# Kernel optimization log

Measured on AMD Instinct MI355X. Metric: run time of the kernel, lower is better.

Reference implementation:

```python
import jax, jax.numpy as jnp
import numpy as np

TAU_MEM = 0.02
THRESHOLD = 0.5
RESET_POTENTIAL = 0.0
SURROGATE_BETA = 4.0
LN_EPS = 1e-6

B, T, F_IN, F_OUT = 64, 1024, 512, 512


def fast_sigmoid(x, beta):
    # Continuous fast-sigmoid surrogate spike: 0.5 * (beta*x / (1 + beta*|x|)) + 0.5
    bx = beta * x
    return 0.5 * bx / (1.0 + jnp.abs(bx)) + 0.5


def setup_inputs() -> dict:
    key = jax.random.key(0)
    k1, k2, k3 = jax.random.split(key, 3)
    spikes = jax.random.uniform(k1, (B, T, F_IN), dtype=jnp.float32)
    W = jax.random.normal(k2, (F_IN, F_OUT), dtype=jnp.float32) / np.sqrt(F_IN)
    b = jnp.zeros((F_OUT,), dtype=jnp.float32)
    ln_scale = jnp.ones((F_OUT,), dtype=jnp.float32)
    ln_bias = jnp.zeros((F_OUT,), dtype=jnp.float32)
    return {"spikes": spikes, "W": W, "b": b, "ln_scale": ln_scale, "ln_bias": ln_bias}


def reference(spikes, W, b, ln_scale, ln_bias):
    # Dense projection of input spike trains: [B,T,F_in] -> [B,T,F_out]
    currents = jnp.einsum('bti,io->bto', spikes, W) + b

    alpha = jnp.exp(jnp.float32(-1.0 / TAU_MEM))

    def lif_step(v_mem, cur):
        v_mem = alpha * v_mem + (1.0 - alpha) * cur
        spike = fast_sigmoid(v_mem - THRESHOLD, SURROGATE_BETA)
        v_mem = v_mem * (1.0 - spike) + RESET_POTENTIAL * spike
        return v_mem, spike

    v0 = jnp.zeros((spikes.shape[0], W.shape[1]), dtype=currents.dtype)
    _, out = jax.lax.scan(lif_step, v0, jnp.transpose(currents, (1, 0, 2)))  # [T,B,F]
    out = jnp.transpose(out, (1, 0, 2))  # [B,T,F]

    # LayerNorm over last axis (flax defaults: eps=1e-6, scale & bias)
    mean = jnp.mean(out, axis=-1, keepdims=True)
    var = jnp.var(out, axis=-1, keepdims=True)
    out = (out - mean) * jax.lax.rsqrt(var + LN_EPS) * ln_scale + ln_bias
    return out
```

## Files before the change

kernel.cpp:

```cpp
#include <hip/hip_runtime.h>

#define THREADS 1024
#define NBLK 512
#define BUFSZ 49152

typedef _Float16 half8 __attribute__((ext_vector_type(8)));
typedef float floatx4 __attribute__((ext_vector_type(4)));

__global__ void wcvt_kernel(const float* __restrict__ W, unsigned short* __restrict__ Wt) {
  __shared__ float tile[32][33];
  const int tx = threadIdx.x, ty = threadIdx.y;
  const int nb = blockIdx.x * 32, kb = blockIdx.y * 32;
#pragma unroll
  for (int i = 0; i < 4; ++i)
    tile[ty + 8 * i][tx] = W[(size_t)(kb + ty + 8 * i) * 512 + nb + tx];
  __syncthreads();
#pragma unroll
  for (int i = 0; i < 4; ++i) {
    union { _Float16 h; unsigned short u; } v;
    v.h = (_Float16)tile[tx][ty + 8 * i];
    Wt[(size_t)(nb + ty + 8 * i) * 512 + kb + tx] = v.u;
  }
}

__global__ __launch_bounds__(THREADS, 4) void lif_fused_kernel(
    const float* __restrict__ A, const unsigned short* __restrict__ Wt,
    const float* __restrict__ bias, const float* __restrict__ lnw,
    const float* __restrict__ lnb, float* __restrict__ out) {
  __shared__ uint4 smem4[9216];
  unsigned char* smem = (unsigned char*)smem4;

  const int tid  = threadIdx.x;
  const int lane = tid & 63;
  const int wave = tid >> 6;
  const int wrow = wave >> 2;
  const int wcol = wave & 3;
  const int l15  = lane & 15;
  const int g    = lane >> 4;
  const int rowBase = blockIdx.x * 128;

  const int arow = tid >> 3;
  const float* asrc =
      A + (size_t)(rowBase + arow) * 512 + ((tid & 7) ^ (arow & 7)) * 4;
  const int brow = tid >> 2;
  const unsigned short* bsrc =
      Wt + (size_t)brow * 512 + ((tid & 3) ^ (brow & 3) ^ ((brow >> 2) & 3)) * 8;

  auto stage = [&](int buf, int c) {
    int offA = buf * BUFSZ + wave * 1024;
    offA = __builtin_amdgcn_readfirstlane(offA);
    __builtin_amdgcn_global_load_lds(
        (const __attribute__((address_space(1))) void*)(asrc + c * 32),
        (__attribute__((address_space(3))) void*)(smem + offA), 16, 0, 0);
    int offB = buf * BUFSZ + 16384 + wave * 1024;
    offB = __builtin_amdgcn_readfirstlane(offB);
    __builtin_amdgcn_global_load_lds(
        (const __attribute__((address_space(1))) void*)(bsrc + c * 32),
        (__attribute__((address_space(3))) void*)(smem + offB), 16, 0, 0);
    __builtin_amdgcn_global_load_lds(
        (const __attribute__((address_space(1))) void*)(bsrc + 256 * 512 + c * 32),
        (__attribute__((address_space(3))) void*)(smem + offB + 16384), 16, 0, 0);
  };

  const int aRB = (wrow * 32 + l15) * 128;
  const int aO0 = (((g << 1) ^ (l15 & 7)) << 4);
  const int aO1 = aO0 ^ 16;
  const int bRB = 16384 + (wcol * 128 + l15) * 64 +
                  ((g ^ (l15 & 3) ^ ((l15 >> 2) & 3)) << 4);

  floatx4 acc[2][8];
#pragma unroll
  for (int m = 0; m < 2; ++m)
#pragma unroll
    for (int n = 0; n < 8; ++n)
      acc[m][n] = (floatx4){0.f, 0.f, 0.f, 0.f};

  auto mk = [](float4 lo, float4 hi) {
    half8 t;
    t[0] = (_Float16)lo.x; t[1] = (_Float16)lo.y;
    t[2] = (_Float16)lo.z; t[3] = (_Float16)lo.w;
    t[4] = (_Float16)hi.x; t[5] = (_Float16)hi.y;
    t[6] = (_Float16)hi.z; t[7] = (_Float16)hi.w;
    return t;
  };

  stage(0, 0);
  stage(1, 1);
  stage(2, 2);

#pragma unroll
  for (int c = 0; c < 16; ++c) {
    if (c < 14) {
      asm volatile("s_waitcnt vmcnt(6)" ::: "memory");
    } else if (c == 14) {
      asm volatile("s_waitcnt vmcnt(3)" ::: "memory");
    } else {
      asm volatile("s_waitcnt vmcnt(0)" ::: "memory");
    }
    __builtin_amdgcn_s_barrier();
    __builtin_amdgcn_sched_barrier(0);

    const int buf = c % 3;
    const unsigned char* ab = smem + buf * BUFSZ + aRB;
    half8 a0 = mk(*(const float4*)(ab + aO0), *(const float4*)(ab + aO1));
    half8 a1 = mk(*(const float4*)(ab + 2048 + aO0), *(const float4*)(ab + 2048 + aO1));
    const unsigned char* bb = smem + buf * BUFSZ + bRB;
    __builtin_amdgcn_s_setprio(1);
#pragma unroll
    for (int n = 0; n < 8; ++n) {
      half8 bf = *(const half8*)(bb + n * 1024);
      acc[0][n] = __builtin_amdgcn_mfma_f32_16x16x32_f16(a0, bf, acc[0][n], 0, 0, 0);
      acc[1][n] = __builtin_amdgcn_mfma_f32_16x16x32_f16(a1, bf, acc[1][n], 0, 0, 0);
    }
    __builtin_amdgcn_s_setprio(0);
    __builtin_amdgcn_sched_barrier(0);
    __builtin_amdgcn_s_barrier();
    __builtin_amdgcn_sched_barrier(0);
    if (c < 13) stage(buf, c + 3);
  }
  __syncthreads();

  float bcol[8], lsc[8], lbc[8];
#pragma unroll
  for (int n = 0; n < 8; ++n) {
    const int col = wcol * 128 + n * 16 + l15;
    bcol[n] = bias[col];
    lsc[n]  = lnw[col];
    lbc[n]  = lnb[col];
  }
#pragma unroll
  for (int m = 0; m < 2; ++m)
#pragma unroll
    for (int n = 0; n < 8; ++n)
#pragma unroll
      for (int r = 0; r < 4; ++r) {
        float x  = acc[m][n][r] + bcol[n] - 0.5f;
        float bx = 4.0f * x;
        acc[m][n][r] = 0.5f * bx / (1.0f + fabsf(bx)) + 0.5f;
      }

  float rs[2][4], rq[2][4];
#pragma unroll
  for (int m = 0; m < 2; ++m)
#pragma unroll
    for (int r = 0; r < 4; ++r) {
      float s = 0.f, q = 0.f;
#pragma unroll
      for (int n = 0; n < 8; ++n) {
        float v = acc[m][n][r];
        s += v;
        q += v * v;
      }
      rs[m][r] = s;
      rq[m][r] = q;
    }
#pragma unroll
  for (int d = 1; d < 16; d <<= 1) {
#pragma unroll
    for (int m = 0; m < 2; ++m)
#pragma unroll
      for (int r = 0; r < 4; ++r) {
        rs[m][r] += __shfl_xor(rs[m][r], d, 16);
        rq[m][r] += __shfl_xor(rq[m][r], d, 16);
      }
  }

  float* redS = (float*)smem4;
  float* redQ = redS + 512;
  float* mv   = redQ + 512;
  if (l15 == 0) {
#pragma unroll
    for (int m = 0; m < 2; ++m)
#pragma unroll
      for (int r = 0; r < 4; ++r) {
        const int row = wrow * 32 + m * 16 + g * 4 + r;
        redS[row * 4 + wcol] = rs[m][r];
        redQ[row * 4 + wcol] = rq[m][r];
      }
  }
  __syncthreads();
  if (tid < 128) {
    const float S = redS[tid * 4] + redS[tid * 4 + 1] + redS[tid * 4 + 2] + redS[tid * 4 + 3];
    const float Q = redQ[tid * 4] + redQ[tid * 4 + 1] + redQ[tid * 4 + 2] + redQ[tid * 4 + 3];
    const float mean = S * (1.0f / 512.0f);
    const float var  = Q * (1.0f / 512.0f) - mean * mean;
    mv[tid * 2]     = mean;
    mv[tid * 2 + 1] = rsqrtf(var + 1e-6f);
  }
  __syncthreads();

#pragma unroll
  for (int m = 0; m < 2; ++m)
#pragma unroll
    for (int r = 0; r < 4; ++r) {
      const int row  = wrow * 32 + m * 16 + g * 4 + r;
      const float mean = mv[row * 2];
      const float rstd = mv[row * 2 + 1];
      const size_t base = (size_t)(rowBase + row) * 512;
#pragma unroll
      for (int n = 0; n < 8; ++n) {
        const int col = wcol * 128 + n * 16 + l15;
        out[base + col] = (acc[m][n][r] - mean) * rstd * lsc[n] + lbc[n];
      }
    }
}

extern "C" void kernel_launch(void* const* d_in, const int* in_sizes, int n_in,
                              void* d_out, int out_size, void* d_ws, size_t ws_size,
                              hipStream_t stream) {
  const float* spikes = (const float*)d_in[0];
  const float* W      = (const float*)d_in[1];
  const float* b      = (const float*)d_in[2];
  const float* lnw    = (const float*)d_in[3];
  const float* lnb    = (const float*)d_in[4];
  float* out = (float*)d_out;
  unsigned short* Wt = (unsigned short*)d_ws;

  wcvt_kernel<<<dim3(16, 16), dim3(32, 8), 0, stream>>>(W, Wt);
  lif_fused_kernel<<<NBLK, THREADS, 0, stream>>>(spikes, Wt, b, lnw, lnb, out);
}
```

Measured before the change: 94.80 us.

## Halve block threads, double per-wave M tile, interleave staged loads with MFMA phases

Block size drops from 1024 to 512 threads, so each wave now computes 64x128 of output instead of 32x128, doubling the accumulator registers. Each K step is split into four MFMA phases separated by barriers, with the next stage's A and B global-to-LDS loads issued in pieces between them. Pipelining depth goes from three chunks in flight to a prefetch distance of two inside a three-buffer ring. The aim is more register-level reuse of A and B fragments per LDS read and better overlap of loads with math. In exchange it raises VGPR pressure, halves occupancy bounds, and adds more barriers per iteration.

Result: faster. 89.58 us (-5.5%).

```diff
diff --git a/kernel.cpp b/kernel.cpp
--- a/kernel.cpp
+++ b/kernel.cpp
@@ -1,8 +1,9 @@
 #include <hip/hip_runtime.h>
 
-#define THREADS 1024
+#define THREADS 512
 #define NBLK 512
 #define BUFSZ 49152
+#define BOFF 16384
 
 typedef _Float16 half8 __attribute__((ext_vector_type(8)));
 typedef float floatx4 __attribute__((ext_vector_type(4)));
@@ -23,7 +24,7 @@
   }
 }
 
-__global__ __launch_bounds__(THREADS, 4) void lif_fused_kernel(
+__global__ __launch_bounds__(THREADS, 2) void lif_fused_kernel(
     const float* __restrict__ A, const unsigned short* __restrict__ Wt,
     const float* __restrict__ bias, const float* __restrict__ lnw,
     const float* __restrict__ lnb, float* __restrict__ out) {
@@ -39,38 +40,42 @@
   const int g    = lane >> 4;
   const int rowBase = blockIdx.x * 128;
 
-  const int arow = tid >> 3;
+  const int ar = tid >> 3;
   const float* asrc =
-      A + (size_t)(rowBase + arow) * 512 + ((tid & 7) ^ (arow & 7)) * 4;
-  const int brow = tid >> 2;
-  const unsigned short* bsrc =
-      Wt + (size_t)brow * 512 + ((tid & 3) ^ (brow & 3) ^ ((brow >> 2) & 3)) * 8;
-
-  auto stage = [&](int buf, int c) {
-    int offA = buf * BUFSZ + wave * 1024;
-    offA = __builtin_amdgcn_readfirstlane(offA);
+      A + (size_t)(rowBase + ar) * 512 + (((tid & 7) ^ (ar & 7)) << 2);
+  const int sB = (tid & 3) ^ ((tid >> 2) & 3) ^ ((tid >> 4) & 3);
+  const unsigned short* bsrc = Wt + (size_t)(tid >> 2) * 512 + sB * 8;
+
+  auto stageA = [&](int buf, int c) {
+    int o0 = buf * BUFSZ + wave * 1024;
+    o0 = __builtin_amdgcn_readfirstlane(o0);
     __builtin_amdgcn_global_load_lds(
         (const __attribute__((address_space(1))) void*)(asrc + c * 32),
-        (__attribute__((address_space(3))) void*)(smem + offA), 16, 0, 0);
-    int offB = buf * BUFSZ + 16384 + wave * 1024;
-    offB = __builtin_amdgcn_readfirstlane(offB);
+        (__attribute__((address_space(3))) void*)(smem + o0), 16, 0, 0);
+    int o1 = buf * BUFSZ + 8192 + wave * 1024;
+    o1 = __builtin_amdgcn_readfirstlane(o1);
     __builtin_amdgcn_global_load_lds(
-        (const __attribute__((address_space(1))) void*)(bsrc + c * 32),
-        (__attribute__((address_space(3))) void*)(smem + offB), 16, 0, 0);
-    __builtin_amdgcn_global_load_lds(
-        (const __attribute__((address_space(1))) void*)(bsrc + 256 * 512 + c * 32),
-        (__attribute__((address_space(3))) void*)(smem + offB + 16384), 16, 0, 0);
+        (const __attribute__((address_space(1))) void*)(asrc + 32768 + c * 32),
+        (__attribute__((address_space(3))) void*)(smem + o1), 16, 0, 0);
   };
-
-  const int aRB = (wrow * 32 + l15) * 128;
-  const int aO0 = (((g << 1) ^ (l15 & 7)) << 4);
-  const int aO1 = aO0 ^ 16;
-  const int bRB = 16384 + (wcol * 128 + l15) * 64 +
-                  ((g ^ (l15 & 3) ^ ((l15 >> 2) & 3)) << 4);
-
-  floatx4 acc[2][8];
-#pragma unroll
-  for (int m = 0; m < 2; ++m)
+  auto stageB = [&](int buf, int c, int i0) {
+#pragma unroll
+    for (int i = 0; i < 2; ++i) {
+      int o = buf * BUFSZ + BOFF + (i0 + i) * 8192 + wave * 1024;
+      o = __builtin_amdgcn_readfirstlane(o);
+      __builtin_amdgcn_global_load_lds(
+          (const __attribute__((address_space(1))) void*)(bsrc + (i0 + i) * 65536 + c * 32),
+          (__attribute__((address_space(3))) void*)(smem + o), 16, 0, 0);
+    }
+  };
+
+  const int aBase = (wrow * 64 + l15) * 128 + (((2 * g) ^ (l15 & 7)) << 4);
+  const int bBase = BOFF + (wcol * 128 + l15) * 64 +
+                    ((g ^ (l15 & 3) ^ ((l15 >> 2) & 3)) << 4);
+
+  floatx4 acc[4][8];
+#pragma unroll
+  for (int m = 0; m < 4; ++m)
 #pragma unroll
     for (int n = 0; n < 8; ++n)
       acc[m][n] = (floatx4){0.f, 0.f, 0.f, 0.f};
@@ -84,16 +89,13 @@
     return t;
   };
 
-  stage(0, 0);
-  stage(1, 1);
-  stage(2, 2);
+  stageA(0, 0); stageB(0, 0, 0); stageB(0, 0, 2);
+  stageA(1, 1); stageB(1, 1, 0); stageB(1, 1, 2);
 
 #pragma unroll
   for (int c = 0; c < 16; ++c) {
-    if (c < 14) {
+    if (c < 15) {
       asm volatile("s_waitcnt vmcnt(6)" ::: "memory");
-    } else if (c == 14) {
-      asm volatile("s_waitcnt vmcnt(3)" ::: "memory");
     } else {
       asm volatile("s_waitcnt vmcnt(0)" ::: "memory");
     }
@@ -101,22 +103,85 @@
     __builtin_amdgcn_sched_barrier(0);
 
     const int buf = c % 3;
-    const unsigned char* ab = smem + buf * BUFSZ + aRB;
-    half8 a0 = mk(*(const float4*)(ab + aO0), *(const float4*)(ab + aO1));
-    half8 a1 = mk(*(const float4*)(ab + 2048 + aO0), *(const float4*)(ab + 2048 + aO1));
-    const unsigned char* bb = smem + buf * BUFSZ + bRB;
-    __builtin_amdgcn_s_setprio(1);
-#pragma unroll
-    for (int n = 0; n < 8; ++n) {
-      half8 bf = *(const half8*)(bb + n * 1024);
-      acc[0][n] = __builtin_amdgcn_mfma_f32_16x16x32_f16(a0, bf, acc[0][n], 0, 0, 0);
-      acc[1][n] = __builtin_amdgcn_mfma_f32_16x16x32_f16(a1, bf, acc[1][n], 0, 0, 0);
-    }
-    __builtin_amdgcn_s_setprio(0);
-    __builtin_amdgcn_sched_barrier(0);
-    __builtin_amdgcn_s_barrier();
-    __builtin_amdgcn_sched_barrier(0);
-    if (c < 13) stage(buf, c + 3);
+    const int nbuf = (c + 2) % 3;
+    const unsigned char* base = smem + buf * BUFSZ;
+
+    half8 a0, a1, b0, b1, b2, b3;
+    {
+      int o = aBase;
+      a0 = mk(*(const float4*)(base + o), *(const float4*)(base + (o ^ 16)));
+      o = aBase + 2048;
+      a1 = mk(*(const float4*)(base + o), *(const float4*)(base + (o ^ 16)));
+    }
+    b0 = *(const half8*)(base + bBase);
+    b1 = *(const half8*)(base + bBase + 1024);
+    b2 = *(const half8*)(base + bBase + 2048);
+    b3 = *(const half8*)(base + bBase + 3072);
+    if (c < 14) stageA(nbuf, c + 2);
+    __builtin_amdgcn_s_setprio(1);
+    acc[0][0] = __builtin_amdgcn_mfma_f32_16x16x32_f16(a0, b0, acc[0][0], 0, 0, 0);
+    acc[1][0] = __builtin_amdgcn_mfma_f32_16x16x32_f16(a1, b0, acc[1][0], 0, 0, 0);
+    acc[0][1] = __builtin_amdgcn_mfma_f32_16x16x32_f16(a0, b1, acc[0][1], 0, 0, 0);
+    acc[1][1] = __builtin_amdgcn_mfma_f32_16x16x32_f16(a1, b1, acc[1][1], 0, 0, 0);
+    acc[0][2] = __builtin_amdgcn_mfma_f32_16x16x32_f16(a0, b2, acc[0][2], 0, 0, 0);
+    acc[1][2] = __builtin_amdgcn_mfma_f32_16x16x32_f16(a1, b2, acc[1][2], 0, 0, 0);
+    acc[0][3] = __builtin_amdgcn_mfma_f32_16x16x32_f16(a0, b3, acc[0][3], 0, 0, 0);
+    acc[1][3] = __builtin_amdgcn_mfma_f32_16x16x32_f16(a1, b3, acc[1][3], 0, 0, 0);
+    __builtin_amdgcn_s_setprio(0);
+    __builtin_amdgcn_s_barrier();
+    __builtin_amdgcn_sched_barrier(0);
+
+    half8 b4, b5, b6, b7;
+    b4 = *(const half8*)(base + bBase + 4096);
+    b5 = *(const half8*)(base + bBase + 5120);
+    b6 = *(const half8*)(base + bBase + 6144);
+    b7 = *(const half8*)(base + bBase + 7168);
+    if (c < 14) stageB(nbuf, c + 2, 0);
+    __builtin_amdgcn_s_setprio(1);
+    acc[0][4] = __builtin_amdgcn_mfma_f32_16x16x32_f16(a0, b4, acc[0][4], 0, 0, 0);
+    acc[1][4] = __builtin_amdgcn_mfma_f32_16x16x32_f16(a1, b4, acc[1][4], 0, 0, 0);
+    acc[0][5] = __builtin_amdgcn_mfma_f32_16x16x32_f16(a0, b5, acc[0][5], 0, 0, 0);
+    acc[1][5] = __builtin_amdgcn_mfma_f32_16x16x32_f16(a1, b5, acc[1][5], 0, 0, 0);
+    acc[0][6] = __builtin_amdgcn_mfma_f32_16x16x32_f16(a0, b6, acc[0][6], 0, 0, 0);
+    acc[1][6] = __builtin_amdgcn_mfma_f32_16x16x32_f16(a1, b6, acc[1][6], 0, 0, 0);
+    acc[0][7] = __builtin_amdgcn_mfma_f32_16x16x32_f16(a0, b7, acc[0][7], 0, 0, 0);
+    acc[1][7] = __builtin_amdgcn_mfma_f32_16x16x32_f16(a1, b7, acc[1][7], 0, 0, 0);
+    __builtin_amdgcn_s_setprio(0);
+    __builtin_amdgcn_s_barrier();
+    __builtin_amdgcn_sched_barrier(0);
+
+    half8 a2, a3;
+    {
+      int o = aBase + 4096;
+      a2 = mk(*(const float4*)(base + o), *(const float4*)(base + (o ^ 16)));
+      o = aBase + 6144;
+      a3 = mk(*(const float4*)(base + o), *(const float4*)(base + (o ^ 16)));
+    }
+    if (c < 14) stageB(nbuf, c + 2, 2);
+    __builtin_amdgcn_s_setprio(1);
+    acc[2][4] = __builtin_amdgcn_mfma_f32_16x16x32_f16(a2, b4, acc[2][4], 0, 0, 0);
+    acc[3][4] = __builtin_amdgcn_mfma_f32_16x16x32_f16(a3, b4, acc[3][4], 0, 0, 0);
+    acc[2][5] = __builtin_amdgcn_mfma_f32_16x16x32_f16(a2, b5, acc[2][5], 0, 0, 0);
+    acc[3][5] = __builtin_amdgcn_mfma_f32_16x16x32_f16(a3, b5, acc[3][5], 0, 0, 0);
+    acc[2][6] = __builtin_amdgcn_mfma_f32_16x16x32_f16(a2, b6, acc[2][6], 0, 0, 0);
+    acc[3][6] = __builtin_amdgcn_mfma_f32_16x16x32_f16(a3, b6, acc[3][6], 0, 0, 0);
+    acc[2][7] = __builtin_amdgcn_mfma_f32_16x16x32_f16(a2, b7, acc[2][7], 0, 0, 0);
+    acc[3][7] = __builtin_amdgcn_mfma_f32_16x16x32_f16(a3, b7, acc[3][7], 0, 0, 0);
+    __builtin_amdgcn_s_setprio(0);
+    __builtin_amdgcn_s_barrier();
+    __builtin_amdgcn_sched_barrier(0);
+
+    __builtin_amdgcn_s_setprio(1);
+    acc[2][0] = __builtin_amdgcn_mfma_f32_16x16x32_f16(a2, b0, acc[2][0], 0, 0, 0);
+    acc[3][0] = __builtin_amdgcn_mfma_f32_16x16x32_f16(a3, b0, acc[3][0], 0, 0, 0);
+    acc[2][1] = __builtin_amdgcn_mfma_f32_16x16x32_f16(a2, b1, acc[2][1], 0, 0, 0);
+    acc[3][1] = __builtin_amdgcn_mfma_f32_16x16x32_f16(a3, b1, acc[3][1], 0, 0, 0);
+    acc[2][2] = __builtin_amdgcn_mfma_f32_16x16x32_f16(a2, b2, acc[2][2], 0, 0, 0);
+    acc[3][2] = __builtin_amdgcn_mfma_f32_16x16x32_f16(a3, b2, acc[3][2], 0, 0, 0);
+    acc[2][3] = __builtin_amdgcn_mfma_f32_16x16x32_f16(a2, b3, acc[2][3], 0, 0, 0);
+    acc[3][3] = __builtin_amdgcn_mfma_f32_16x16x32_f16(a3, b3, acc[3][3], 0, 0, 0);
+    __builtin_amdgcn_s_setprio(0);
+    __builtin_amdgcn_sched_barrier(0);
   }
   __syncthreads();
 
@@ -129,7 +194,7 @@
     lbc[n]  = lnb[col];
   }
 #pragma unroll
-  for (int m = 0; m < 2; ++m)
+  for (int m = 0; m < 4; ++m)
 #pragma unroll
     for (int n = 0; n < 8; ++n)
 #pragma unroll
@@ -139,9 +204,9 @@
         acc[m][n][r] = 0.5f * bx / (1.0f + fabsf(bx)) + 0.5f;
       }
 
-  float rs[2][4], rq[2][4];
-#pragma unroll
-  for (int m = 0; m < 2; ++m)
+  float rs[4][4], rq[4][4];
+#pragma unroll
+  for (int m = 0; m < 4; ++m)
 #pragma unroll
     for (int r = 0; r < 4; ++r) {
       float s = 0.f, q = 0.f;
@@ -157,7 +222,7 @@
 #pragma unroll
   for (int d = 1; d < 16; d <<= 1) {
 #pragma unroll
-    for (int m = 0; m < 2; ++m)
+    for (int m = 0; m < 4; ++m)
 #pragma unroll
       for (int r = 0; r < 4; ++r) {
         rs[m][r] += __shfl_xor(rs[m][r], d, 16);
@@ -170,10 +235,10 @@
   float* mv   = redQ + 512;
   if (l15 == 0) {
 #pragma unroll
-    for (int m = 0; m < 2; ++m)
+    for (int m = 0; m < 4; ++m)
 #pragma unroll
       for (int r = 0; r < 4; ++r) {
-        const int row = wrow * 32 + m * 16 + g * 4 + r;
+        const int row = wrow * 64 + m * 16 + g * 4 + r;
         redS[row * 4 + wcol] = rs[m][r];
         redQ[row * 4 + wcol] = rq[m][r];
       }
@@ -190,10 +255,10 @@
   __syncthreads();
 
 #pragma unroll
-  for (int m = 0; m < 2; ++m)
+  for (int m = 0; m < 4; ++m)
 #pragma unroll
     for (int r = 0; r < 4; ++r) {
-      const int row  = wrow * 32 + m * 16 + g * 4 + r;
+      const int row  = wrow * 64 + m * 16 + g * 4 + r;
       const float mean = mv[row * 2];
       const float rstd = mv[row * 2 + 1];
       const size_t base = (size_t)(rowBase + row) * 512;
```

## Halve block tile to 64 rows, double-buffer with fragment-ordered LDS layout

Applied to the files above, without the earlier changes.

Blocks shrink from 1024 to 512 threads covering 64 rows each, and the grid doubles to 1024 blocks. The triple buffer becomes a double buffer. Global-to-LDS loads now write data already in MFMA fragment order, so the XOR swizzle is gone. All A/B fragments are read into registers before a barrier, and the next stage is issued before the MFMAs so loads overlap compute. This aims for better occupancy and latency hiding, at the cost of each block re-reading the whole W tile, which doubles W traffic, and a shallower prefetch.

Result: slower. 130.5 us (+37.7%).

```diff
diff --git a/kernel.cpp b/kernel.cpp
--- a/kernel.cpp
+++ b/kernel.cpp
@@ -1,8 +1,9 @@
 #include <hip/hip_runtime.h>
 
-#define THREADS 1024
-#define NBLK 512
-#define BUFSZ 49152
+#define THREADS 512
+#define NBLK 1024
+#define BUFSZ 40960
+#define BOFF 8192
 
 typedef _Float16 half8 __attribute__((ext_vector_type(8)));
 typedef float floatx4 __attribute__((ext_vector_type(4)));
@@ -27,7 +28,7 @@
     const float* __restrict__ A, const unsigned short* __restrict__ Wt,
     const float* __restrict__ bias, const float* __restrict__ lnw,
     const float* __restrict__ lnb, float* __restrict__ out) {
-  __shared__ uint4 smem4[9216];
+  __shared__ uint4 smem4[5120];
   unsigned char* smem = (unsigned char*)smem4;
 
   const int tid  = threadIdx.x;
@@ -37,36 +38,31 @@
   const int wcol = wave & 3;
   const int l15  = lane & 15;
   const int g    = lane >> 4;
-  const int rowBase = blockIdx.x * 128;
-
-  const int arow = tid >> 3;
-  const float* asrc =
-      A + (size_t)(rowBase + arow) * 512 + ((tid & 7) ^ (arow & 7)) * 4;
-  const int brow = tid >> 2;
-  const unsigned short* bsrc =
-      Wt + (size_t)brow * 512 + ((tid & 3) ^ (brow & 3) ^ ((brow >> 2) & 3)) * 8;
+  const int rowBase = blockIdx.x * 64;
+
+  const int aRowS = (wave >> 2) * 32 + ((wave >> 1) & 1) * 16 + l15;
+  const float* asrc = A + (size_t)(rowBase + aRowS) * 512 + g * 8 + (wave & 1) * 4;
+  const unsigned short* bsrc0 =
+      Wt + (size_t)((wave >> 1) * 128 + (wave & 1) * 64 + l15) * 512 + g * 8;
 
   auto stage = [&](int buf, int c) {
-    int offA = buf * BUFSZ + wave * 1024;
-    offA = __builtin_amdgcn_readfirstlane(offA);
+    int oA = buf * BUFSZ + wave * 1024;
+    oA = __builtin_amdgcn_readfirstlane(oA);
     __builtin_amdgcn_global_load_lds(
         (const __attribute__((address_space(1))) void*)(asrc + c * 32),
-        (__attribute__((address_space(3))) void*)(smem + offA), 16, 0, 0);
-    int offB = buf * BUFSZ + 16384 + wave * 1024;
-    offB = __builtin_amdgcn_readfirstlane(offB);
-    __builtin_amdgcn_global_load_lds(
-        (const __attribute__((address_space(1))) void*)(bsrc + c * 32),
-        (__attribute__((address_space(3))) void*)(smem + offB), 16, 0, 0);
-    __builtin_amdgcn_global_load_lds(
-        (const __attribute__((address_space(1))) void*)(bsrc + 256 * 512 + c * 32),
-        (__attribute__((address_space(3))) void*)(smem + offB + 16384), 16, 0, 0);
+        (__attribute__((address_space(3))) void*)(smem + oA), 16, 0, 0);
+#pragma unroll
+    for (int i = 0; i < 4; ++i) {
+      int oB = buf * BUFSZ + BOFF + (wave * 4 + i) * 1024;
+      oB = __builtin_amdgcn_readfirstlane(oB);
+      __builtin_amdgcn_global_load_lds(
+          (const __attribute__((address_space(1))) void*)(bsrc0 + (size_t)i * 16 * 512 + c * 32),
+          (__attribute__((address_space(3))) void*)(smem + oB), 16, 0, 0);
+    }
   };
 
-  const int aRB = (wrow * 32 + l15) * 128;
-  const int aO0 = (((g << 1) ^ (l15 & 7)) << 4);
-  const int aO1 = aO0 ^ 16;
-  const int bRB = 16384 + (wcol * 128 + l15) * 64 +
-                  ((g ^ (l15 & 3) ^ ((l15 >> 2) & 3)) << 4);
+  const int aRd = wrow * 4096 + lane * 16;
+  const int bRd = BOFF + wcol * 8192 + lane * 16;
 
   floatx4 acc[2][8];
 #pragma unroll
@@ -86,37 +82,55 @@
 
   stage(0, 0);
   stage(1, 1);
-  stage(2, 2);
 
 #pragma unroll
   for (int c = 0; c < 16; ++c) {
-    if (c < 14) {
-      asm volatile("s_waitcnt vmcnt(6)" ::: "memory");
-    } else if (c == 14) {
-      asm volatile("s_waitcnt vmcnt(3)" ::: "memory");
+    if (c < 15) {
+      asm volatile("s_waitcnt vmcnt(5)" ::: "memory");
     } else {
       asm volatile("s_waitcnt vmcnt(0)" ::: "memory");
     }
     __builtin_amdgcn_s_barrier();
     __builtin_amdgcn_sched_barrier(0);
 
-    const int buf = c % 3;
-    const unsigned char* ab = smem + buf * BUFSZ + aRB;
-    half8 a0 = mk(*(const float4*)(ab + aO0), *(const float4*)(ab + aO1));
-    half8 a1 = mk(*(const float4*)(ab + 2048 + aO0), *(const float4*)(ab + 2048 + aO1));
-    const unsigned char* bb = smem + buf * BUFSZ + bRB;
+    const unsigned char* base = smem + (c & 1) * BUFSZ;
+    half8 a0 = mk(*(const float4*)(base + aRd),
+                  *(const float4*)(base + aRd + 1024));
+    half8 a1 = mk(*(const float4*)(base + aRd + 2048),
+                  *(const float4*)(base + aRd + 3072));
+    half8 b0 = *(const half8*)(base + bRd);
+    half8 b1 = *(const half8*)(base + bRd + 1024);
+    half8 b2 = *(const half8*)(base + bRd + 2048);
+    half8 b3 = *(const half8*)(base + bRd + 3072);
+    half8 b4 = *(const half8*)(base + bRd + 4096);
+    half8 b5 = *(const half8*)(base + bRd + 5120);
+    half8 b6 = *(const half8*)(base + bRd + 6144);
+    half8 b7 = *(const half8*)(base + bRd + 7168);
+    asm volatile("s_waitcnt lgkmcnt(0)" ::: "memory");
+    __builtin_amdgcn_sched_barrier(0);
+    __builtin_amdgcn_s_barrier();
+    __builtin_amdgcn_sched_barrier(0);
+    if (c < 14) stage(c & 1, c + 2);
+
     __builtin_amdgcn_s_setprio(1);
-#pragma unroll
-    for (int n = 0; n < 8; ++n) {
-      half8 bf = *(const half8*)(bb + n * 1024);
-      acc[0][n] = __builtin_amdgcn_mfma_f32_16x16x32_f16(a0, bf, acc[0][n], 0, 0, 0);
-      acc[1][n] = __builtin_amdgcn_mfma_f32_16x16x32_f16(a1, bf, acc[1][n], 0, 0, 0);
-    }
+    acc[0][0] = __builtin_amdgcn_mfma_f32_16x16x32_f16(a0, b0, acc[0][0], 0, 0, 0);
+    acc[1][0] = __builtin_amdgcn_mfma_f32_16x16x32_f16(a1, b0, acc[1][0], 0, 0, 0);
+    acc[0][1] = __builtin_amdgcn_mfma_f32_16x16x32_f16(a0, b1, acc[0][1], 0, 0, 0);
+    acc[1][1] = __builtin_amdgcn_mfma_f32_16x16x32_f16(a1, b1, acc[1][1], 0, 0, 0);
+    acc[0][2] = __builtin_amdgcn_mfma_f32_16x16x32_f16(a0, b2, acc[0][2], 0, 0, 0);
+    acc[1][2] = __builtin_amdgcn_mfma_f32_16x16x32_f16(a1, b2, acc[1][2], 0, 0, 0);
+    acc[0][3] = __builtin_amdgcn_mfma_f32_16x16x32_f16(a0, b3, acc[0][3], 0, 0, 0);
+    acc[1][3] = __builtin_amdgcn_mfma_f32_16x16x32_f16(a1, b3, acc[1][3], 0, 0, 0);
+    acc[0][4] = __builtin_amdgcn_mfma_f32_16x16x32_f16(a0, b4, acc[0][4], 0, 0, 0);
+    acc[1][4] = __builtin_amdgcn_mfma_f32_16x16x32_f16(a1, b4, acc[1][4], 0, 0, 0);
+    acc[0][5] = __builtin_amdgcn_mfma_f32_16x16x32_f16(a0, b5, acc[0][5], 0, 0, 0);
+    acc[1][5] = __builtin_amdgcn_mfma_f32_16x16x32_f16(a1, b5, acc[1][5], 0, 0, 0);
+    acc[0][6] = __builtin_amdgcn_mfma_f32_16x16x32_f16(a0, b6, acc[0][6], 0, 0, 0);
+    acc[1][6] = __builtin_amdgcn_mfma_f32_16x16x32_f16(a1, b6, acc[1][6], 0, 0, 0);
+    acc[0][7] = __builtin_amdgcn_mfma_f32_16x16x32_f16(a0, b7, acc[0][7], 0, 0, 0);
+    acc[1][7] = __builtin_amdgcn_mfma_f32_16x16x32_f16(a1, b7, acc[1][7], 0, 0, 0);
     __builtin_amdgcn_s_setprio(0);
     __builtin_amdgcn_sched_barrier(0);
-    __builtin_amdgcn_s_barrier();
-    __builtin_amdgcn_sched_barrier(0);
-    if (c < 13) stage(buf, c + 3);
   }
   __syncthreads();
 
@@ -166,8 +180,8 @@
   }
 
   float* redS = (float*)smem4;
-  float* redQ = redS + 512;
-  float* mv   = redQ + 512;
+  float* redQ = redS + 256;
+  float* mv   = redQ + 256;
   if (l15 == 0) {
 #pragma unroll
     for (int m = 0; m < 2; ++m)
@@ -179,7 +193,7 @@
       }
   }
   __syncthreads();
-  if (tid < 128) {
+  if (tid < 64) {
     const float S = redS[tid * 4] + redS[tid * 4 + 1] + redS[tid * 4 + 2] + redS[tid * 4 + 3];
     const float Q = redQ[tid * 4] + redQ[tid * 4 + 1] + redQ[tid * 4 + 2] + redQ[tid * 4 + 3];
     const float mean = S * (1.0f / 512.0f);
```
